# Performance work log

Measured on AMD Instinct MI355X. Metric: run time of the kernel, lower is better.

Reference implementation:

```python
import jax, jax.numpy as jnp
import numpy as np

H = 256  # hidden_dim


def _bidir_lstm_layer(x, W_ih, W_hh, bias):
    """x: [S, B, in]; W_ih: [2, in, 4H]; W_hh: [2, H, 4H]; bias: [2, 4H].
    Returns [S, B, 2H] (forward || backward outputs per timestep).
    PyTorch gate order: i, f, g, o."""
    B = x.shape[1]
    init = (jnp.zeros((B, H), x.dtype), jnp.zeros((B, H), x.dtype))
    # precompute input projections for the whole sequence, both directions
    xp = jnp.einsum('sbi,dij->dsbj', x, W_ih) + bias[:, None, None, :]  # [2,S,B,4H]

    def make_step(W_hh_d):
        def step(carry, xt):
            h, c = carry
            g = xt + h @ W_hh_d  # [B, 4H]
            i = jax.nn.sigmoid(g[:, :H])
            f = jax.nn.sigmoid(g[:, H:2 * H])
            gg = jnp.tanh(g[:, 2 * H:3 * H])
            o = jax.nn.sigmoid(g[:, 3 * H:])
            c = f * c + i * gg
            h = o * jnp.tanh(c)
            return (h, c), h
        return step

    _, h_f = jax.lax.scan(make_step(W_hh[0]), init, xp[0])
    _, h_b = jax.lax.scan(make_step(W_hh[1]), init, xp[1], reverse=True)
    return jnp.concatenate([h_f, h_b], axis=-1)  # [S, B, 2H]


def setup_inputs() -> dict:
    key = jax.random.key(0)
    ks = jax.random.split(key, 11)
    s = 0.05  # small init scale to keep gates in their dynamic range
    inp = {
        'x': jax.random.normal(ks[0], (8192, 1024), jnp.float32),
        'w_ih0': jax.random.normal(ks[1], (2, 1024, 4 * H), jnp.float32) * s,
        'w_hh0': jax.random.normal(ks[2], (2, H, 4 * H), jnp.float32) * s,
        'b0': jax.random.normal(ks[3], (2, 4 * H), jnp.float32) * s,
        'w_ih': jax.random.normal(ks[4], (4, 2, 2 * H, 4 * H), jnp.float32) * s,
        'w_hh': jax.random.normal(ks[5], (4, 2, H, 4 * H), jnp.float32) * s,
        'b': jax.random.normal(ks[6], (4, 2, 4 * H), jnp.float32) * s,
        'w1': jax.random.normal(ks[7], (2 * H, 32), jnp.float32) * s,
        'b1': jax.random.normal(ks[8], (32,), jnp.float32) * s,
        'w2': jax.random.normal(ks[9], (32, 2), jnp.float32) * s,
        'b2': jax.random.normal(ks[10], (2,), jnp.float32) * s,
    }
    return inp


def reference(x, w_ih0, w_hh0, b0, w_ih, w_hh, b, w1, b1, w2, b2):
    # x: [S, 1024] -> [S, B=1, 1024] (module does unsqueeze(0).transpose(0,1))
    h = x[:, None, :]
    h = _bidir_lstm_layer(h, w_ih0, w_hh0, b0)
    for l in range(4):  # layers 1..4 (fixed count)
        h = _bidir_lstm_layer(h, w_ih[l], w_hh[l], b[l])
    # cat(forward output at last step, backward output at first step)
    feat = jnp.concatenate([h[-1, :, :H], h[0, :, H:]], axis=1)  # [1, 2H]
    out = (feat @ w1 + b1) @ w2 + b2  # [1, 2]
    return out
```

## Files before the change

### kernel.cpp

```cpp
#include <hip/hip_runtime.h>

constexpr int SQ = 8192;
constexpr int HD = 256;
constexpr int NG = 1024;

typedef __fp16 h2 __attribute__((ext_vector_type(2)));
typedef unsigned int uint;

__device__ __forceinline__ float sigm_f(float x) {
  float e = __builtin_amdgcn_exp2f(-1.4426950408889634f * x);
  return __builtin_amdgcn_rcpf(1.0f + e);
}
__device__ __forceinline__ float tanh_f(float x) {
  float e = __builtin_amdgcn_exp2f(2.885390081777927f * x);
  return 1.0f - 2.0f * __builtin_amdgcn_rcpf(1.0f + e);
}

__global__ __launch_bounds__(256) void gemm_xp(const float* __restrict__ A, int K,
                                               const float* __restrict__ W,
                                               const float* __restrict__ bias,
                                               float* __restrict__ out) {
  __shared__ float Al[16][64];
  __shared__ float Bl[16][64];
  const int tid = threadIdx.x;
  const int bm = blockIdx.x * 64;
  const int d  = blockIdx.y >> 4;
  const int bn = (blockIdx.y & 15) * 64;
  const float* Wd = W + (size_t)d * K * NG;
  const float* bd = bias + (size_t)d * NG;
  float* outd = out + (size_t)d * SQ * NG;

  const int m4 = (tid >> 4) << 2;
  const int n4 = (tid & 15) << 2;
  const int am = tid >> 2, ak = (tid & 3) << 2;
  const int bk = tid >> 4, bnn = (tid & 15) << 2;

  float acc[4][4] = {};
  for (int kt = 0; kt < K; kt += 16) {
    float4 av = *(const float4*)(A + (size_t)(bm + am) * K + kt + ak);
    float4 bv = *(const float4*)(Wd + (size_t)(kt + bk) * NG + bn + bnn);
    __syncthreads();
    Al[ak + 0][am] = av.x;
    Al[ak + 1][am] = av.y;
    Al[ak + 2][am] = av.z;
    Al[ak + 3][am] = av.w;
    *(float4*)&Bl[bk][bnn] = bv;
    __syncthreads();
#pragma unroll
    for (int k = 0; k < 16; ++k) {
      float4 a = *(const float4*)&Al[k][m4];
      float4 b = *(const float4*)&Bl[k][n4];
      float ar[4] = {a.x, a.y, a.z, a.w};
      float br[4] = {b.x, b.y, b.z, b.w};
#pragma unroll
      for (int i = 0; i < 4; ++i)
#pragma unroll
        for (int jj = 0; jj < 4; ++jj)
          acc[i][jj] = fmaf(ar[i], br[jj], acc[i][jj]);
    }
  }
#pragma unroll
  for (int i = 0; i < 4; ++i) {
    float4 o;
    o.x = acc[i][0] + bd[bn + n4 + 0];
    o.y = acc[i][1] + bd[bn + n4 + 1];
    o.z = acc[i][2] + bd[bn + n4 + 2];
    o.w = acc[i][3] + bd[bn + n4 + 3];
    *(float4*)(outd + (size_t)(bm + m4 + i) * NG + bn + n4) = o;
  }
}

__global__ __launch_bounds__(1024, 4) void lstm_rec(const float* __restrict__ Whh,
                                                    const float* __restrict__ xp,
                                                    float* __restrict__ obuf) {
  __shared__ uint4 wlds[9 * 1024];
  __shared__ float glds[1024];
  __shared__ uint4 hlds[32];
  const int d = blockIdx.x;
  const int j = threadIdx.x;
  const float* W = Whh + (size_t)d * HD * NG;
  const float* xpd = xp + (size_t)d * SQ * NG;

  h2 wreg[92];
#pragma unroll
  for (int r = 0; r < 92; ++r)
    wreg[r] = __builtin_amdgcn_cvt_pkrtz(W[(size_t)(2 * r) * NG + j],
                                         W[(size_t)(2 * r + 1) * NG + j]);
#pragma unroll
  for (int q8 = 0; q8 < 9; ++q8) {
    const int base = 184 + 8 * q8;
    uint4 v;
    v.x = __builtin_bit_cast(uint, __builtin_amdgcn_cvt_pkrtz(W[(size_t)(base + 0) * NG + j], W[(size_t)(base + 1) * NG + j]));
    v.y = __builtin_bit_cast(uint, __builtin_amdgcn_cvt_pkrtz(W[(size_t)(base + 2) * NG + j], W[(size_t)(base + 3) * NG + j]));
    v.z = __builtin_bit_cast(uint, __builtin_amdgcn_cvt_pkrtz(W[(size_t)(base + 4) * NG + j], W[(size_t)(base + 5) * NG + j]));
    v.w = __builtin_bit_cast(uint, __builtin_amdgcn_cvt_pkrtz(W[(size_t)(base + 6) * NG + j], W[(size_t)(base + 7) * NG + j]));
    wlds[q8 * 1024 + j] = v;
  }
  if (j < 32) hlds[j] = make_uint4(0u, 0u, 0u, 0u);
  __syncthreads();

  const int fwd = (d == 0) ? 1 : 0;
  int t = fwd ? 0 : SQ - 1;
  const int dt = fwd ? 1 : -1;
  const int qg = j >> 8;
  const int u = j & 255;
  float c = 0.0f;
  float xp_cur = xpd[(size_t)t * NG + j];

  for (int step = 0; step < SQ; ++step) {
    float xp_next = (step + 1 < SQ) ? xpd[(size_t)(t + dt) * NG + j] : 0.0f;

    float a0 = xp_cur, a1 = 0.0f;
#pragma unroll
    for (int cq = 0; cq < 23; ++cq) {
      uint4 hq = hlds[cq];
      a0 = __builtin_amdgcn_fdot2(wreg[4 * cq + 0], __builtin_bit_cast(h2, hq.x), a0, false);
      a1 = __builtin_amdgcn_fdot2(wreg[4 * cq + 1], __builtin_bit_cast(h2, hq.y), a1, false);
      a0 = __builtin_amdgcn_fdot2(wreg[4 * cq + 2], __builtin_bit_cast(h2, hq.z), a0, false);
      a1 = __builtin_amdgcn_fdot2(wreg[4 * cq + 3], __builtin_bit_cast(h2, hq.w), a1, false);
    }
#pragma unroll
    for (int q8 = 0; q8 < 9; ++q8) {
      uint4 wq = wlds[q8 * 1024 + j];
      uint4 hq = hlds[23 + q8];
      a0 = __builtin_amdgcn_fdot2(__builtin_bit_cast(h2, wq.x), __builtin_bit_cast(h2, hq.x), a0, false);
      a1 = __builtin_amdgcn_fdot2(__builtin_bit_cast(h2, wq.y), __builtin_bit_cast(h2, hq.y), a1, false);
      a0 = __builtin_amdgcn_fdot2(__builtin_bit_cast(h2, wq.z), __builtin_bit_cast(h2, hq.z), a0, false);
      a1 = __builtin_amdgcn_fdot2(__builtin_bit_cast(h2, wq.w), __builtin_bit_cast(h2, hq.w), a1, false);
    }
    float acc = a0 + a1;

    float act = (qg == 2) ? tanh_f(acc) : sigm_f(acc);
    glds[j] = act;
    __syncthreads();

    if (qg == 0) {
      float iv = glds[u];
      float fv = glds[256 + u];
      float gv = glds[512 + u];
      float ov = glds[768 + u];
      c = fv * c + iv * gv;
      float hv = ov * tanh_f(c);
      obuf[(size_t)t * 512 + (d << 8) + u] = hv;
      float hn = __shfl_down(hv, 1);
      if (!(u & 1)) {
        h2 p = __builtin_amdgcn_cvt_pkrtz(hv, hn);
        ((uint*)hlds)[u >> 1] = __builtin_bit_cast(uint, p);
      }
    }
    __syncthreads();
    xp_cur = xp_next;
    t += dt;
  }
}

__global__ void cls_k(const float* __restrict__ buf, const float* __restrict__ w1,
                      const float* __restrict__ b1, const float* __restrict__ w2,
                      const float* __restrict__ b2, float* __restrict__ out) {
  __shared__ float feat[512];
  __shared__ float hid[32];
  const int t = threadIdx.x;
  feat[t] = (t < 256) ? buf[(size_t)(SQ - 1) * 512 + t] : buf[t];
  __syncthreads();
  if (t < 32) {
    float a = b1[t];
    for (int k = 0; k < 512; ++k) a = fmaf(feat[k], w1[k * 32 + t], a);
    hid[t] = a;
  }
  __syncthreads();
  if (t < 2) {
    float a = b2[t];
    for (int k = 0; k < 32; ++k) a = fmaf(hid[k], w2[k * 2 + t], a);
    out[t] = a;
  }
}

extern "C" void kernel_launch(void* const* d_in, const int* in_sizes, int n_in,
                              void* d_out, int out_size, void* d_ws, size_t ws_size,
                              hipStream_t stream) {
  const float* x     = (const float*)d_in[0];
  const float* w_ih0 = (const float*)d_in[1];
  const float* w_hh0 = (const float*)d_in[2];
  const float* b0    = (const float*)d_in[3];
  const float* w_ih  = (const float*)d_in[4];
  const float* w_hh  = (const float*)d_in[5];
  const float* b     = (const float*)d_in[6];
  const float* w1    = (const float*)d_in[7];
  const float* b1    = (const float*)d_in[8];
  const float* w2    = (const float*)d_in[9];
  const float* b2    = (const float*)d_in[10];

  float* xp   = (float*)d_ws;
  float* bufA = xp + (size_t)2 * SQ * NG;
  float* bufB = bufA + (size_t)SQ * 512;

  const dim3 ggrid(SQ / 64, 32);

  gemm_xp<<<ggrid, 256, 0, stream>>>(x, 1024, w_ih0, b0, xp);
  lstm_rec<<<2, 1024, 0, stream>>>(w_hh0, xp, bufA);

  float* cur = bufA;
  float* nxt = bufB;
  for (int l = 0; l < 4; ++l) {
    gemm_xp<<<ggrid, 256, 0, stream>>>(cur, 512, w_ih + (size_t)l * 2 * 512 * 1024,
                                       b + (size_t)l * 2 * 1024, xp);
    lstm_rec<<<2, 1024, 0, stream>>>(w_hh + (size_t)l * 2 * 256 * 1024, xp, nxt);
    float* tmp = cur; cur = nxt; nxt = tmp;
  }

  cls_k<<<1, 512, 0, stream>>>(cur, w1, b1, w2, b2, (float*)d_out);
}
```

Before: 77.28 ms.

## Split each LSTM direction across two workgroups with global-memory flag handshake

Each direction's recurrence now runs on two workgroups, each computing half of the gate columns. All recurrent weights fit in registers because each thread holds half a column's K-range and a cross-lane shuffle sums the two halves, which removes the LDS weight reads. Activations are exchanged between the paired workgroups every timestep through global memory, using release/acquire flags and a spin-wait. This adds a cross-CU synchronization round trip per step on the serial critical path, and it depends on both workgroups of a pair being resident at the same time.

```diff
diff --git a/kernel.cpp b/kernel.cpp
--- a/kernel.cpp
+++ b/kernel.cpp
@@ -70,83 +70,89 @@
   }
 }
 
-__global__ __launch_bounds__(1024, 4) void lstm_rec(const float* __restrict__ Whh,
-                                                    const float* __restrict__ xp,
-                                                    float* __restrict__ obuf) {
-  __shared__ uint4 wlds[9 * 1024];
-  __shared__ float glds[1024];
+__global__ void init_flags(int* flags) {
+  if (threadIdx.x < 4) flags[threadIdx.x] = 0;
+}
+
+__global__ __launch_bounds__(1024, 4) void lstm_rec2(const float* __restrict__ Whh,
+                                                     const float* __restrict__ xp,
+                                                     float* __restrict__ obuf,
+                                                     float* gx, int* flags, int ep) {
+  __shared__ float glds[512];
   __shared__ uint4 hlds[32];
-  const int d = blockIdx.x;
+  const int b = blockIdx.x;
+  const int d = b >> 1, g = b & 1;
   const int j = threadIdx.x;
-  const float* W = Whh + (size_t)d * HD * NG;
+  const int w = j >> 6, l = j & 63;
+  const int cl = w * 32 + (l & 31);
+  const int s  = l >> 5;
+  const int gc = g * 512 + cl;
+  const float* W   = Whh + (size_t)d * HD * NG;
   const float* xpd = xp + (size_t)d * SQ * NG;
-
-  h2 wreg[92];
-#pragma unroll
-  for (int r = 0; r < 92; ++r)
-    wreg[r] = __builtin_amdgcn_cvt_pkrtz(W[(size_t)(2 * r) * NG + j],
-                                         W[(size_t)(2 * r + 1) * NG + j]);
-#pragma unroll
-  for (int q8 = 0; q8 < 9; ++q8) {
-    const int base = 184 + 8 * q8;
-    uint4 v;
-    v.x = __builtin_bit_cast(uint, __builtin_amdgcn_cvt_pkrtz(W[(size_t)(base + 0) * NG + j], W[(size_t)(base + 1) * NG + j]));
-    v.y = __builtin_bit_cast(uint, __builtin_amdgcn_cvt_pkrtz(W[(size_t)(base + 2) * NG + j], W[(size_t)(base + 3) * NG + j]));
-    v.z = __builtin_bit_cast(uint, __builtin_amdgcn_cvt_pkrtz(W[(size_t)(base + 4) * NG + j], W[(size_t)(base + 5) * NG + j]));
-    v.w = __builtin_bit_cast(uint, __builtin_amdgcn_cvt_pkrtz(W[(size_t)(base + 6) * NG + j], W[(size_t)(base + 7) * NG + j]));
-    wlds[q8 * 1024 + j] = v;
-  }
+  float* gx_self  = gx + ((size_t)(d * 2 + g)) * 2 * 512;
+  float* gx_other = gx + ((size_t)(d * 2 + (1 - g))) * 2 * 512;
+  int* flag_self  = flags + d * 2 + g;
+  int* flag_other = flags + d * 2 + (1 - g);
+
+  h2 wreg[64];
+  const float* Wc = W + (size_t)(s * 128) * NG + gc;
+#pragma unroll
+  for (int k = 0; k < 64; ++k)
+    wreg[k] = __builtin_amdgcn_cvt_pkrtz(Wc[(size_t)(2 * k) * NG],
+                                         Wc[(size_t)(2 * k + 1) * NG]);
+
   if (j < 32) hlds[j] = make_uint4(0u, 0u, 0u, 0u);
   __syncthreads();
 
   const int fwd = (d == 0) ? 1 : 0;
   int t = fwd ? 0 : SQ - 1;
   const int dt = fwd ? 1 : -1;
-  const int qg = j >> 8;
-  const int u = j & 255;
-  float c = 0.0f;
-  float xp_cur = xpd[(size_t)t * NG + j];
+  const int hbase = s * 16;
+  const bool is_tanh = (g == 1) && (cl < 256);
+  float cc = 0.0f;
+  float xp_cur = xpd[(size_t)t * NG + gc];
 
   for (int step = 0; step < SQ; ++step) {
-    float xp_next = (step + 1 < SQ) ? xpd[(size_t)(t + dt) * NG + j] : 0.0f;
-
-    float a0 = xp_cur, a1 = 0.0f;
-#pragma unroll
-    for (int cq = 0; cq < 23; ++cq) {
-      uint4 hq = hlds[cq];
-      a0 = __builtin_amdgcn_fdot2(wreg[4 * cq + 0], __builtin_bit_cast(h2, hq.x), a0, false);
-      a1 = __builtin_amdgcn_fdot2(wreg[4 * cq + 1], __builtin_bit_cast(h2, hq.y), a1, false);
-      a0 = __builtin_amdgcn_fdot2(wreg[4 * cq + 2], __builtin_bit_cast(h2, hq.z), a0, false);
-      a1 = __builtin_amdgcn_fdot2(wreg[4 * cq + 3], __builtin_bit_cast(h2, hq.w), a1, false);
-    }
-#pragma unroll
-    for (int q8 = 0; q8 < 9; ++q8) {
-      uint4 wq = wlds[q8 * 1024 + j];
-      uint4 hq = hlds[23 + q8];
-      a0 = __builtin_amdgcn_fdot2(__builtin_bit_cast(h2, wq.x), __builtin_bit_cast(h2, hq.x), a0, false);
-      a1 = __builtin_amdgcn_fdot2(__builtin_bit_cast(h2, wq.y), __builtin_bit_cast(h2, hq.y), a1, false);
-      a0 = __builtin_amdgcn_fdot2(__builtin_bit_cast(h2, wq.z), __builtin_bit_cast(h2, hq.z), a0, false);
-      a1 = __builtin_amdgcn_fdot2(__builtin_bit_cast(h2, wq.w), __builtin_bit_cast(h2, hq.w), a1, false);
-    }
-    float acc = a0 + a1;
-
-    float act = (qg == 2) ? tanh_f(acc) : sigm_f(acc);
-    glds[j] = act;
-    __syncthreads();
-
-    if (qg == 0) {
-      float iv = glds[u];
-      float fv = glds[256 + u];
-      float gv = glds[512 + u];
-      float ov = glds[768 + u];
-      c = fv * c + iv * gv;
-      float hv = ov * tanh_f(c);
-      obuf[(size_t)t * 512 + (d << 8) + u] = hv;
+    float xp_next = (step + 1 < SQ) ? xpd[(size_t)(t + dt) * NG + gc] : 0.0f;
+
+    float a0 = 0.0f, a1 = 0.0f;
+#pragma unroll
+    for (int q = 0; q < 16; ++q) {
+      uint4 hq = hlds[hbase + q];
+      a0 = __builtin_amdgcn_fdot2(wreg[4 * q + 0], __builtin_bit_cast(h2, hq.x), a0, false);
+      a1 = __builtin_amdgcn_fdot2(wreg[4 * q + 1], __builtin_bit_cast(h2, hq.y), a1, false);
+      a0 = __builtin_amdgcn_fdot2(wreg[4 * q + 2], __builtin_bit_cast(h2, hq.z), a0, false);
+      a1 = __builtin_amdgcn_fdot2(wreg[4 * q + 3], __builtin_bit_cast(h2, hq.w), a1, false);
+    }
+    float part = a0 + a1;
+    float full = part + __shfl_xor(part, 32);
+    float pre  = full + xp_cur;
+    float act  = is_tanh ? tanh_f(pre) : sigm_f(pre);
+
+    float* gxs = gx_self + (step & 1) * 512;
+    if (l < 32) {
+      glds[cl] = act;
+      __hip_atomic_store(gxs + cl, act, __ATOMIC_RELAXED, __HIP_MEMORY_SCOPE_AGENT);
+    }
+    __syncthreads();
+
+    if (j < 256) {
+      const int target = ep + step + 1;
+      if (j == 0)
+        __hip_atomic_store(flag_self, target, __ATOMIC_RELEASE, __HIP_MEMORY_SCOPE_AGENT);
+      while (__hip_atomic_load(flag_other, __ATOMIC_ACQUIRE, __HIP_MEMORY_SCOPE_AGENT) < target) {}
+      const float* gxo = gx_other + (step & 1) * 512;
+      float o0 = __hip_atomic_load(gxo + j,       __ATOMIC_RELAXED, __HIP_MEMORY_SCOPE_AGENT);
+      float o1 = __hip_atomic_load(gxo + 256 + j, __ATOMIC_RELAXED, __HIP_MEMORY_SCOPE_AGENT);
+      float iv, fv, gv, ov;
+      if (g == 0) { iv = glds[j]; fv = glds[256 + j]; gv = o0; ov = o1; }
+      else        { gv = glds[j]; ov = glds[256 + j]; iv = o0; fv = o1; }
+      cc = fv * cc + iv * gv;
+      float hv = ov * tanh_f(cc);
+      if (g == 0) obuf[(size_t)t * 512 + (d << 8) + j] = hv;
       float hn = __shfl_down(hv, 1);
-      if (!(u & 1)) {
-        h2 p = __builtin_amdgcn_cvt_pkrtz(hv, hn);
-        ((uint*)hlds)[u >> 1] = __builtin_bit_cast(uint, p);
-      }
+      if (!(j & 1))
+        ((uint*)hlds)[j >> 1] = __builtin_bit_cast(uint, __builtin_amdgcn_cvt_pkrtz(hv, hn));
     }
     __syncthreads();
     xp_cur = xp_next;
@@ -193,18 +199,23 @@
   float* xp   = (float*)d_ws;
   float* bufA = xp + (size_t)2 * SQ * NG;
   float* bufB = bufA + (size_t)SQ * 512;
+  float* gx   = bufB + (size_t)SQ * 512;
+  int*   flags = (int*)(gx + 2 * 2 * 2 * 512);
 
   const dim3 ggrid(SQ / 64, 32);
 
+  init_flags<<<1, 64, 0, stream>>>(flags);
+
   gemm_xp<<<ggrid, 256, 0, stream>>>(x, 1024, w_ih0, b0, xp);
-  lstm_rec<<<2, 1024, 0, stream>>>(w_hh0, xp, bufA);
+  lstm_rec2<<<4, 1024, 0, stream>>>(w_hh0, xp, bufA, gx, flags, 0 * SQ);
 
   float* cur = bufA;
   float* nxt = bufB;
-  for (int l = 0; l < 4; ++l) {
-    gemm_xp<<<ggrid, 256, 0, stream>>>(cur, 512, w_ih + (size_t)l * 2 * 512 * 1024,
-                                       b + (size_t)l * 2 * 1024, xp);
-    lstm_rec<<<2, 1024, 0, stream>>>(w_hh + (size_t)l * 2 * 256 * 1024, xp, nxt);
+  for (int lyr = 0; lyr < 4; ++lyr) {
+    gemm_xp<<<ggrid, 256, 0, stream>>>(cur, 512, w_ih + (size_t)lyr * 2 * 512 * 1024,
+                                       b + (size_t)lyr * 2 * 1024, xp);
+    lstm_rec2<<<4, 1024, 0, stream>>>(w_hh + (size_t)lyr * 2 * 256 * 1024, xp, nxt,
+                                      gx, flags, (lyr + 1) * SQ);
     float* tmp = cur; cur = nxt; nxt = tmp;
   }
 
```

Result: slower. 116.0 ms (+50.1%).
